# Kernel optimization log

Hardware: AMD Instinct MI355X
Metric: run time of the kernel (lower is better)

## Reference

```python
import jax, jax.numpy as jnp
import numpy as np

N_ENT = 50000
N_REL = 16
N_BASES = 8
H_DIM = 128
N_EDGES = 800000


def setup_inputs() -> dict:
    key = jax.random.key(0)
    ks = jax.random.split(key, 12)
    s = 1.0 / np.sqrt(H_DIM)
    inp = {
        "entity_emb": jax.random.normal(ks[0], (N_ENT, H_DIM), jnp.float32) * s,
        "basis1": jax.random.normal(ks[1], (N_BASES, H_DIM, H_DIM), jnp.float32) * s,
        "w_comp1": jax.random.normal(ks[2], (N_REL, N_BASES), jnp.float32) * (1.0 / np.sqrt(N_BASES)),
        "loop_w1": jax.random.normal(ks[3], (H_DIM, H_DIM), jnp.float32) * s,
        "bias1": jnp.zeros((H_DIM,), jnp.float32),
        "basis2": jax.random.normal(ks[4], (N_BASES, H_DIM, H_DIM), jnp.float32) * s,
        "w_comp2": jax.random.normal(ks[5], (N_REL, N_BASES), jnp.float32) * (1.0 / np.sqrt(N_BASES)),
        "loop_w2": jax.random.normal(ks[6], (H_DIM, H_DIM), jnp.float32) * s,
        "bias2": jnp.zeros((H_DIM,), jnp.float32),
        "src": jax.random.randint(ks[7], (N_EDGES,), 0, N_ENT, jnp.int32),
        "dst": jax.random.randint(ks[8], (N_EDGES,), 0, N_ENT, jnp.int32),
        "rel_type": jax.random.randint(ks[9], (N_EDGES,), 0, N_REL, jnp.int32),
    }
    return inp


def _rgcn_layer(h, src, dst, rel, basis, w_comp, loop_w, bias):
    # Basis decomposition: W_r = sum_b w_comp[r, b] * basis[b]   -> [R, d, d]
    W = jnp.einsum('rb,bio->rio', w_comp, basis)
    # Sum aggregation is linear, so aggregate h[src] per (dst, rel) first,
    # then apply the relation matrix once per (node, rel). Same math as
    # per-edge transform + scatter-add, far less FLOP/traffic.
    seg = dst.astype(jnp.int32) * N_REL + rel.astype(jnp.int32)  # [E]
    agg = jax.ops.segment_sum(h[src], seg, num_segments=N_ENT * N_REL)
    agg = agg.reshape(N_ENT, N_REL, -1)                           # [N, R, d]
    msg = jnp.einsum('nri,rio->no', agg, W)                       # [N, d]
    out = msg + h @ loop_w + bias
    return jax.nn.relu(out)


def reference(entity_emb, basis1, w_comp1, loop_w1, bias1,
              basis2, w_comp2, loop_w2, bias2, src, dst, rel_type):
    # Encoder dropout is identity in eval mode.
    h = _rgcn_layer(entity_emb, src, dst, rel_type, basis1, w_comp1, loop_w1, bias1)
    h = _rgcn_layer(h, src, dst, rel_type, basis2, w_comp2, loop_w2, bias2)
    return h
```

## Files before the change

### kernel.cpp

```cpp
#include <hip/hip_runtime.h>
#include <hip/hip_bf16.h>

#define HDIM 128
#define NREL 16
#define NBASES 8
#define KSLOTS 17
#define KDIM (KSLOTS * HDIM)

typedef short bf16x8 __attribute__((ext_vector_type(8)));
typedef short s16x4 __attribute__((ext_vector_type(4)));
typedef float f32x4 __attribute__((ext_vector_type(4)));

static __device__ __forceinline__ short f2bf(float x) {
    __hip_bfloat16 b = __float2bfloat16(x);
    return *(short*)&b;
}
static __device__ __forceinline__ float bf2f(short u) {
    unsigned v = ((unsigned)(unsigned short)u) << 16;
    return __uint_as_float(v);
}

__global__ void compute_wt(const float* __restrict__ basis,
                           const float* __restrict__ wcomp,
                           short* __restrict__ wtL) {
    int ro = blockIdx.x;
    int r = ro >> 7, o = ro & 127;
    int i = threadIdx.x;
    float acc = 0.f;
#pragma unroll
    for (int b = 0; b < NBASES; ++b)
        acc += wcomp[r * NBASES + b] * basis[(b * HDIM + i) * HDIM + o];
    wtL[(size_t)o * KDIM + r * HDIM + i] = f2bf(acc);
}

__global__ void transposeL(const float* __restrict__ in, short* __restrict__ wtL) {
    int o = blockIdx.x, i = threadIdx.x;
    wtL[(size_t)o * KDIM + NREL * HDIM + i] = f2bf(in[i * HDIM + o]);
}

__global__ void cast_bf16(const float* __restrict__ in, short* __restrict__ out, int n4) {
    for (int i = blockIdx.x * blockDim.x + threadIdx.x; i < n4; i += gridDim.x * blockDim.x) {
        f32x4 v = ((const f32x4*)in)[i];
        s16x4 o;
#pragma unroll
        for (int j = 0; j < 4; ++j) o[j] = f2bf(v[j]);
        ((s16x4*)out)[i] = o;
    }
}

__global__ void zero_i32(int* __restrict__ p, int n) {
    int i = blockIdx.x * blockDim.x + threadIdx.x;
    if (i < n) p[i] = 0;
}

__global__ __launch_bounds__(256) void hist_k(const int* __restrict__ dst,
                                              const int* __restrict__ rel, int n,
                                              int* __restrict__ hist) {
    for (int i = blockIdx.x * blockDim.x + threadIdx.x; i < n; i += gridDim.x * blockDim.x)
        atomicAdd(&hist[dst[i] * NREL + rel[i]], 1);
}

__global__ __launch_bounds__(1024) void scan_p1(const int* __restrict__ hist, int n,
                                                int* __restrict__ off, int* __restrict__ part) {
    __shared__ int sh[1024];
    int t = threadIdx.x, b = blockIdx.x;
    int i = b * 1024 + t;
    int x = (i < n) ? hist[i] : 0;
    sh[t] = x;
    __syncthreads();
    for (int d = 1; d < 1024; d <<= 1) {
        int v = sh[t];
        int u = (t >= d) ? sh[t - d] : 0;
        __syncthreads();
        sh[t] = v + u;
        __syncthreads();
    }
    if (i < n) off[i] = sh[t] - x;
    if (t == 1023) part[b] = sh[t];
}

__global__ __launch_bounds__(1024) void scan_p2(int* __restrict__ part, int nb) {
    __shared__ int sh[1024];
    int t = threadIdx.x;
    int x = (t < nb) ? part[t] : 0;
    sh[t] = x;
    __syncthreads();
    for (int d = 1; d < 1024; d <<= 1) {
        int v = sh[t];
        int u = (t >= d) ? sh[t - d] : 0;
        __syncthreads();
        sh[t] = v + u;
        __syncthreads();
    }
    if (t < nb) part[t] = sh[t] - x;
}

__global__ __launch_bounds__(1024) void scan_p3(int* __restrict__ off, const int* __restrict__ part,
                                                int n, int nk, int* __restrict__ cur) {
    int i = blockIdx.x * 1024 + threadIdx.x;
    if (i < n) {
        int v = off[i] + part[blockIdx.x];
        off[i] = v;
        if (i < nk) cur[i] = v;
    }
}

__global__ __launch_bounds__(256) void scatter_k(const int* __restrict__ src,
                                                 const int* __restrict__ dst,
                                                 const int* __restrict__ rel, int n,
                                                 int* __restrict__ cur,
                                                 int* __restrict__ edge2) {
    for (int i = blockIdx.x * blockDim.x + threadIdx.x; i < n; i += gridDim.x * blockDim.x) {
        int k = dst[i] * NREL + rel[i];
        int p = atomicAdd(&cur[k], 1);
        edge2[p] = (src[i] & 0xFFFF) | (rel[i] << 16);
    }
}

__global__ __launch_bounds__(256) void agg_build(
    const short* __restrict__ h,
    const int* __restrict__ off,
    const int* __restrict__ edge2,
    short* __restrict__ AGG,
    unsigned short* __restrict__ srcs,
    int c0, int rows) {
    int tid = threadIdx.x;
    int grp = blockIdx.x * 16 + (tid >> 4);
    int lane16 = tid & 15;
    int lane = tid & 63;
    int gb = lane & 48;
    int drow = grp >> 1;
    if (drow >= rows) return;
    int rh = (grp & 1) * 8;
    int d = c0 + drow;
    int kbase = d * NREL + rh;

    int e0 = off[kbase];
    int e8 = off[kbase + 8];
    int deg = e8 - e0;

    int pkv = (e0 + lane16 < e8) ? edge2[e0 + lane16] : 0;

    int rlv[17], srcv[16];
#pragma unroll
    for (int p = 0; p < 16; ++p) {
        int pk = __shfl(pkv, gb + p);
        rlv[p] = (p < deg) ? (((pk >> 16) & 15) - rh) : 255;
        srcv[p] = pk & 0xFFFF;
    }
    rlv[16] = (deg > 16) ? rlv[15] : 255;

    bool single[16];
#pragma unroll
    for (int p = 0; p < 16; ++p)
        single[p] = ((p == 0) || (rlv[p - 1] != rlv[p])) && (rlv[p + 1] != rlv[p]);

    bf16x8 va[16];
#pragma unroll
    for (int p = 0; p < 16; ++p)
        if (p < deg && !single[p])
            va[p] = *(const bf16x8*)(h + (size_t)srcv[p] * HDIM + lane16 * 8);

    unsigned short val = 0xFFFF;
#pragma unroll
    for (int p = 0; p < 16; ++p)
        if (p < deg && rlv[p] == lane16)
            val = single[p] ? (unsigned short)srcv[p] : (unsigned short)0xFFFE;

    float acc[8] = {0.f, 0.f, 0.f, 0.f, 0.f, 0.f, 0.f, 0.f};
    int cs = -1;
    short* outp = AGG + ((size_t)drow * NREL + rh) * HDIM + lane16 * 8;

    auto emit = [&]() {
        bf16x8 o;
#pragma unroll
        for (int c = 0; c < 8; ++c) o[c] = f2bf(acc[c]);
        *(bf16x8*)(outp + cs * HDIM) = o;
    };
    auto take = [&](int sl, bf16x8 v) {
        if (sl != cs) {
            if (cs >= 0) emit();
            cs = sl;
#pragma unroll
            for (int c = 0; c < 8; ++c) acc[c] = 0.f;
        }
#pragma unroll
        for (int c = 0; c < 8; ++c) acc[c] += bf2f(v[c]);
    };

#pragma unroll
    for (int p = 0; p < 16; ++p)
        if (p < deg && !single[p]) take(rlv[p], va[p]);

    for (int e = e0 + 16; e < e8; ++e) {
        int pk = edge2[e];
        int sl = ((pk >> 16) & 15) - rh;
        if (sl == lane16) val = 0xFFFE;
        bf16x8 v = *(const bf16x8*)(h + (size_t)(pk & 0xFFFF) * HDIM + lane16 * 8);
        take(sl, v);
    }
    if (cs >= 0) emit();

    if (lane16 < 8) srcs[(size_t)drow * NREL + rh + lane16] = val;
}

__global__ __launch_bounds__(256, 3) void agg_gemm(
    const short* __restrict__ AGG,
    const short* __restrict__ h,
    const short* __restrict__ wtL,
    const unsigned short* __restrict__ srcs,
    const float* __restrict__ bias,
    short* __restrict__ out_bf,
    float* __restrict__ out_f,
    int c0, int rows) {
    __shared__ short As[64 * HDIM];
    __shared__ short Bs[128 * HDIM];
    int tid = threadIdx.x;
    int row0 = blockIdx.x * 64;
    if (row0 >= rows) return;
    int wave = tid >> 6, lane = tid & 63;
    int mq = (wave & 1) * 32, nq = (wave >> 1) * 64;
    int lr = lane & 15, quad = lane >> 4;

    int r2 = tid >> 2, ca = tid & 3;
    int rb = tid >> 1, cb = (tid & 1) * 8;
    bool ok = (row0 + r2) < rows;

    unsigned wq[8];
    {
        uint4 a = make_uint4(0xFFFFFFFFu, 0xFFFFFFFFu, 0xFFFFFFFFu, 0xFFFFFFFFu);
        uint4 b = a;
        if (ok) {
            const uint4* sp = (const uint4*)(srcs + (size_t)(row0 + r2) * NREL);
            a = sp[0]; b = sp[1];
        }
        wq[0] = a.x; wq[1] = a.y; wq[2] = a.z; wq[3] = a.w;
        wq[4] = b.x; wq[5] = b.y; wq[6] = b.z; wq[7] = b.w;
    }

    bf16x8 apf[4], bpf[8];
    auto loadRegs = [&](int ks) {
        const short* bp = wtL + (size_t)rb * KDIM + ks * HDIM + cb * 8;
#pragma unroll
        for (int j = 0; j < 8; ++j) bpf[j] = *(const bf16x8*)(bp + j * 8);
        if (ks == 16) {
            if (ok) {
                const short* sp = h + (size_t)(c0 + row0 + r2) * HDIM + ca * 32;
#pragma unroll
                for (int j = 0; j < 4; ++j) apf[j] = *(const bf16x8*)(sp + j * 8);
            } else {
#pragma unroll
                for (int j = 0; j < 4; ++j) apf[j] = (bf16x8)0;
            }
        } else {
            unsigned w = 0xFFFFu;
#pragma unroll
            for (int q = 0; q < 8; ++q) if ((ks >> 1) == q) w = wq[q];
            unsigned e = (ks & 1) ? (w >> 16) : (w & 0xFFFFu);
            if (e == 0xFFFFu) {
#pragma unroll
                for (int j = 0; j < 4; ++j) apf[j] = (bf16x8)0;
            } else {
                const short* sp = (e == 0xFFFEu)
                    ? AGG + ((size_t)(row0 + r2) * NREL + ks) * HDIM + ca * 32
                    : h + (size_t)e * HDIM + ca * 32;
#pragma unroll
                for (int j = 0; j < 4; ++j) apf[j] = *(const bf16x8*)(sp + j * 8);
            }
        }
    };
    auto writeLDS = [&]() {
#pragma unroll
        for (int j = 0; j < 4; ++j) {
            int c = ca * 4 + j;
            *(bf16x8*)(As + r2 * HDIM + (c ^ (r2 & 7)) * 8) = apf[j];
        }
#pragma unroll
        for (int j = 0; j < 8; ++j) {
            int c = cb + j;
            *(bf16x8*)(Bs + rb * HDIM + (c ^ (rb & 7)) * 8) = bpf[j];
        }
    };

    f32x4 acc[2][4] = {};

    loadRegs(0);
    writeLDS();
    __syncthreads();

#pragma unroll 1
    for (int ks = 0; ks <= 16; ++ks) {
        if (ks < 16) loadRegs(ks + 1);
#pragma unroll
        for (int kk = 0; kk < 4; ++kk) {
            int c = kk * 4 + quad;
            bf16x8 a[2], b[4];
#pragma unroll
            for (int mi = 0; mi < 2; ++mi) {
                int row = mq + mi * 16 + lr;
                a[mi] = *(const bf16x8*)(As + row * HDIM + (c ^ (row & 7)) * 8);
            }
#pragma unroll
            for (int ni = 0; ni < 4; ++ni) {
                int row = nq + ni * 16 + lr;
                b[ni] = *(const bf16x8*)(Bs + row * HDIM + (c ^ (row & 7)) * 8);
            }
#pragma unroll
            for (int mi = 0; mi < 2; ++mi)
#pragma unroll
                for (int ni = 0; ni < 4; ++ni)
                    acc[mi][ni] = __builtin_amdgcn_mfma_f32_16x16x32_bf16(a[mi], b[ni], acc[mi][ni], 0, 0, 0);
        }
        __syncthreads();
        if (ks < 16) { writeLDS(); __syncthreads(); }
    }

#pragma unroll
    for (int mi = 0; mi < 2; ++mi) {
#pragma unroll
        for (int reg = 0; reg < 4; ++reg) {
            int g = row0 + mq + mi * 16 + quad * 4 + reg;
            if (g < rows) {
                size_t gd = (size_t)(c0 + g) * HDIM;
#pragma unroll
                for (int ni = 0; ni < 4; ++ni) {
                    int n = nq + ni * 16 + lr;
                    float v = acc[mi][ni][reg] + bias[n];
                    v = v > 0.f ? v : 0.f;
                    if (out_bf) out_bf[gd + n] = f2bf(v);
                    else        out_f[gd + n] = v;
                }
            }
        }
    }
}

extern "C" void kernel_launch(void* const* d_in, const int* in_sizes, int n_in,
                              void* d_out, int out_size, void* d_ws, size_t ws_size,
                              hipStream_t stream) {
    const float* emb    = (const float*)d_in[0];
    const float* basis1 = (const float*)d_in[1];
    const float* wc1    = (const float*)d_in[2];
    const float* lw1    = (const float*)d_in[3];
    const float* bias1  = (const float*)d_in[4];
    const float* basis2 = (const float*)d_in[5];
    const float* wc2    = (const float*)d_in[6];
    const float* lw2    = (const float*)d_in[7];
    const float* bias2  = (const float*)d_in[8];
    const int* src = (const int*)d_in[9];
    const int* dst = (const int*)d_in[10];
    const int* rel = (const int*)d_in[11];

    int n_ent = in_sizes[0] / HDIM;
    int n_edges = in_sizes[9];
    int NK = n_ent * NREL;
    int NK1 = NK + 1;

    char* ws = (char*)d_ws;
    size_t wo = 0;
    auto alloc = [&](size_t bytes) {
        void* p = ws + wo;
        wo = (wo + bytes + 255) & ~(size_t)255;
        return p;
    };
    int* hist  = (int*)alloc((size_t)NK1 * 4);
    int* off   = (int*)alloc((size_t)NK1 * 4);
    int* cur   = (int*)alloc((size_t)NK * 4);
    int* part  = (int*)alloc(4096);
    int* edge2 = (int*)alloc((size_t)n_edges * 4);
    short* wtL1 = (short*)alloc((size_t)HDIM * KDIM * 2);
    short* wtL2 = (short*)alloc((size_t)HDIM * KDIM * 2);
    short* h0   = (short*)alloc((size_t)n_ent * HDIM * 2);
    short* h1   = (short*)alloc((size_t)n_ent * HDIM * 2);
    unsigned short* srcs = (unsigned short*)alloc((size_t)n_ent * NREL * 2);

    size_t rowBytes = (size_t)NREL * HDIM * 2;
    size_t avail = (ws_size > wo + rowBytes * 128) ? (ws_size - wo) : rowBytes * 128;
    int CH = (int)(avail / rowBytes);
    if (CH > n_ent) CH = n_ent;
    CH = (CH + 127) & ~127;
    if (CH < 128) CH = 128;
    while ((size_t)CH * rowBytes > avail && CH > 128) CH -= 128;
    short* AGG = (short*)alloc((size_t)CH * rowBytes);

    compute_wt<<<NREL * HDIM, HDIM, 0, stream>>>(basis1, wc1, wtL1);
    compute_wt<<<NREL * HDIM, HDIM, 0, stream>>>(basis2, wc2, wtL2);
    transposeL<<<HDIM, HDIM, 0, stream>>>(lw1, wtL1);
    transposeL<<<HDIM, HDIM, 0, stream>>>(lw2, wtL2);
    cast_bf16<<<512, 256, 0, stream>>>(emb, h0, n_ent * HDIM / 4);

    zero_i32<<<(NK1 + 255) / 256, 256, 0, stream>>>(hist, NK1);
    hist_k<<<1024, 256, 0, stream>>>(dst, rel, n_edges, hist);
    int nsb = (NK1 + 1023) / 1024;
    scan_p1<<<nsb, 1024, 0, stream>>>(hist, NK1, off, part);
    scan_p2<<<1, 1024, 0, stream>>>(part, nsb);
    scan_p3<<<nsb, 1024, 0, stream>>>(off, part, NK1, NK, cur);
    scatter_k<<<1024, 256, 0, stream>>>(src, dst, rel, n_edges, cur, edge2);

    for (int c0 = 0; c0 < n_ent; c0 += CH) {
        int rows = n_ent - c0 < CH ? n_ent - c0 : CH;
        agg_build<<<(rows * 2 + 15) / 16, 256, 0, stream>>>(h0, off, edge2, AGG, srcs, c0, rows);
        agg_gemm<<<(rows + 63) / 64, 256, 0, stream>>>(AGG, h0, wtL1, srcs, bias1,
                                                       h1, nullptr, c0, rows);
    }
    for (int c0 = 0; c0 < n_ent; c0 += CH) {
        int rows = n_ent - c0 < CH ? n_ent - c0 : CH;
        agg_build<<<(rows * 2 + 15) / 16, 256, 0, stream>>>(h1, off, edge2, AGG, srcs, c0, rows);
        agg_gemm<<<(rows + 63) / 64, 256, 0, stream>>>(AGG, h1, wtL2, srcs, bias2,
                                                       nullptr, (float*)d_out, c0, rows);
    }
}
```

Before: 490.8 us.

## Load GEMM operands directly from global memory into MFMA registers, dropping LDS staging

The agg_gemm kernel no longer stages A and B tiles through shared memory with barriers. Each wave now loads its MFMA fragments straight from global memory (h, AGG, or transposed weights) with the K loop fully unrolled, and occupancy is lowered to 2 blocks per CU to make room for the extra registers. This removes LDS writes, LDS reads and __syncthreads, but the weight tile is now fetched redundantly by each wave, and global-load latency is hidden only by unrolling and occupancy. The early return for empty blocks was also dropped, which is safe because every row access is still guarded.

```diff
diff --git a/kernel.cpp b/kernel.cpp
--- a/kernel.cpp
+++ b/kernel.cpp
@@ -204,7 +204,7 @@
     if (lane16 < 8) srcs[(size_t)drow * NREL + rh + lane16] = val;
 }
 
-__global__ __launch_bounds__(256, 3) void agg_gemm(
+__global__ __launch_bounds__(256, 2) void agg_gemm(
     const short* __restrict__ AGG,
     const short* __restrict__ h,
     const short* __restrict__ wtL,
@@ -213,106 +213,72 @@
     short* __restrict__ out_bf,
     float* __restrict__ out_f,
     int c0, int rows) {
-    __shared__ short As[64 * HDIM];
-    __shared__ short Bs[128 * HDIM];
     int tid = threadIdx.x;
     int row0 = blockIdx.x * 64;
-    if (row0 >= rows) return;
     int wave = tid >> 6, lane = tid & 63;
     int mq = (wave & 1) * 32, nq = (wave >> 1) * 64;
     int lr = lane & 15, quad = lane >> 4;
 
-    int r2 = tid >> 2, ca = tid & 3;
-    int rb = tid >> 1, cb = (tid & 1) * 8;
-    bool ok = (row0 + r2) < rows;
-
-    unsigned wq[8];
+    int ra = row0 + mq + lr;
+    int rb = row0 + mq + 16 + lr;
+    bool oka = ra < rows, okb = rb < rows;
+
+    unsigned cA[8], cB[8];
     {
-        uint4 a = make_uint4(0xFFFFFFFFu, 0xFFFFFFFFu, 0xFFFFFFFFu, 0xFFFFFFFFu);
-        uint4 b = a;
-        if (ok) {
-            const uint4* sp = (const uint4*)(srcs + (size_t)(row0 + r2) * NREL);
-            a = sp[0]; b = sp[1];
-        }
-        wq[0] = a.x; wq[1] = a.y; wq[2] = a.z; wq[3] = a.w;
-        wq[4] = b.x; wq[5] = b.y; wq[6] = b.z; wq[7] = b.w;
-    }
-
-    bf16x8 apf[4], bpf[8];
-    auto loadRegs = [&](int ks) {
-        const short* bp = wtL + (size_t)rb * KDIM + ks * HDIM + cb * 8;
-#pragma unroll
-        for (int j = 0; j < 8; ++j) bpf[j] = *(const bf16x8*)(bp + j * 8);
+        uint4 ff = make_uint4(0xFFFFFFFFu, 0xFFFFFFFFu, 0xFFFFFFFFu, 0xFFFFFFFFu);
+        uint4 a0 = ff, a1 = ff, b0 = ff, b1 = ff;
+        if (oka) {
+            const uint4* p = (const uint4*)(srcs + (size_t)ra * NREL);
+            a0 = p[0]; a1 = p[1];
+        }
+        if (okb) {
+            const uint4* p = (const uint4*)(srcs + (size_t)rb * NREL);
+            b0 = p[0]; b1 = p[1];
+        }
+        cA[0] = a0.x; cA[1] = a0.y; cA[2] = a0.z; cA[3] = a0.w;
+        cA[4] = a1.x; cA[5] = a1.y; cA[6] = a1.z; cA[7] = a1.w;
+        cB[0] = b0.x; cB[1] = b0.y; cB[2] = b0.z; cB[3] = b0.w;
+        cB[4] = b1.x; cB[5] = b1.y; cB[6] = b1.z; cB[7] = b1.w;
+    }
+
+    f32x4 acc[2][4] = {};
+    const short* wbase = wtL + (size_t)(nq + lr) * KDIM;
+
+#pragma unroll
+    for (int ks = 0; ks < KSLOTS; ++ks) {
+        const short* pa;
+        const short* pb;
         if (ks == 16) {
-            if (ok) {
-                const short* sp = h + (size_t)(c0 + row0 + r2) * HDIM + ca * 32;
-#pragma unroll
-                for (int j = 0; j < 4; ++j) apf[j] = *(const bf16x8*)(sp + j * 8);
-            } else {
-#pragma unroll
-                for (int j = 0; j < 4; ++j) apf[j] = (bf16x8)0;
-            }
+            pa = oka ? h + (size_t)(c0 + ra) * HDIM : nullptr;
+            pb = okb ? h + (size_t)(c0 + rb) * HDIM : nullptr;
         } else {
-            unsigned w = 0xFFFFu;
-#pragma unroll
-            for (int q = 0; q < 8; ++q) if ((ks >> 1) == q) w = wq[q];
-            unsigned e = (ks & 1) ? (w >> 16) : (w & 0xFFFFu);
-            if (e == 0xFFFFu) {
-#pragma unroll
-                for (int j = 0; j < 4; ++j) apf[j] = (bf16x8)0;
-            } else {
-                const short* sp = (e == 0xFFFEu)
-                    ? AGG + ((size_t)(row0 + r2) * NREL + ks) * HDIM + ca * 32
-                    : h + (size_t)e * HDIM + ca * 32;
-#pragma unroll
-                for (int j = 0; j < 4; ++j) apf[j] = *(const bf16x8*)(sp + j * 8);
-            }
-        }
-    };
-    auto writeLDS = [&]() {
-#pragma unroll
-        for (int j = 0; j < 4; ++j) {
-            int c = ca * 4 + j;
-            *(bf16x8*)(As + r2 * HDIM + (c ^ (r2 & 7)) * 8) = apf[j];
-        }
-#pragma unroll
-        for (int j = 0; j < 8; ++j) {
-            int c = cb + j;
-            *(bf16x8*)(Bs + rb * HDIM + (c ^ (rb & 7)) * 8) = bpf[j];
-        }
-    };
-
-    f32x4 acc[2][4] = {};
-
-    loadRegs(0);
-    writeLDS();
-    __syncthreads();
-
-#pragma unroll 1
-    for (int ks = 0; ks <= 16; ++ks) {
-        if (ks < 16) loadRegs(ks + 1);
+            unsigned ea = (cA[ks >> 1] >> ((ks & 1) * 16)) & 0xFFFFu;
+            unsigned eb = (cB[ks >> 1] >> ((ks & 1) * 16)) & 0xFFFFu;
+            pa = (ea == 0xFFFFu) ? nullptr
+               : (ea == 0xFFFEu) ? AGG + ((size_t)ra * NREL + ks) * HDIM
+                                 : h + (size_t)ea * HDIM;
+            pb = (eb == 0xFFFFu) ? nullptr
+               : (eb == 0xFFFEu) ? AGG + ((size_t)rb * NREL + ks) * HDIM
+                                 : h + (size_t)eb * HDIM;
+        }
+
+        bf16x8 a[4][2], b[4][4];
 #pragma unroll
         for (int kk = 0; kk < 4; ++kk) {
-            int c = kk * 4 + quad;
-            bf16x8 a[2], b[4];
-#pragma unroll
-            for (int mi = 0; mi < 2; ++mi) {
-                int row = mq + mi * 16 + lr;
-                a[mi] = *(const bf16x8*)(As + row * HDIM + (c ^ (row & 7)) * 8);
-            }
-#pragma unroll
-            for (int ni = 0; ni < 4; ++ni) {
-                int row = nq + ni * 16 + lr;
-                b[ni] = *(const bf16x8*)(Bs + row * HDIM + (c ^ (row & 7)) * 8);
-            }
+            int co = kk * 32 + quad * 8;
+            a[kk][0] = pa ? *(const bf16x8*)(pa + co) : (bf16x8)0;
+            a[kk][1] = pb ? *(const bf16x8*)(pb + co) : (bf16x8)0;
+#pragma unroll
+            for (int ni = 0; ni < 4; ++ni)
+                b[kk][ni] = *(const bf16x8*)(wbase + (size_t)ni * 16 * KDIM + ks * HDIM + co);
+        }
+#pragma unroll
+        for (int kk = 0; kk < 4; ++kk)
 #pragma unroll
             for (int mi = 0; mi < 2; ++mi)
 #pragma unroll
                 for (int ni = 0; ni < 4; ++ni)
-                    acc[mi][ni] = __builtin_amdgcn_mfma_f32_16x16x32_bf16(a[mi], b[ni], acc[mi][ni], 0, 0, 0);
-        }
-        __syncthreads();
-        if (ks < 16) { writeLDS(); __syncthreads(); }
+                    acc[mi][ni] = __builtin_amdgcn_mfma_f32_16x16x32_bf16(a[kk][mi], b[kk][ni], acc[mi][ni], 0, 0, 0);
     }
 
 #pragma unroll
```

Measured after the change: 617.6 us. 25.8% more time.
